# Kernel optimization log

Hardware: AMD Instinct MI355X
Metric: run time of the kernel (lower is better)

The kernel has to match this reference:

```python
import jax, jax.numpy as jnp
import numpy as np
import math

B, S, D, H = 4, 2048, 1024, 16
DK = D // H

def setup_inputs() -> dict:
    key = jax.random.key(0)
    ks = jax.random.split(key, 11)
    mk = lambda k, shape: jax.random.normal(k, shape, dtype=jnp.float32)
    inp = {
        'query': mk(ks[0], (B, S, D)),
        'key':   mk(ks[1], (B, S, D)),
        'value': mk(ks[2], (B, S, D)),
        'Wq': mk(ks[3], (D, D)) * 0.02, 'bq': jnp.zeros((D,), jnp.float32),
        'Wk': mk(ks[4], (D, D)) * 0.02, 'bk': jnp.zeros((D,), jnp.float32),
        'Wv': mk(ks[5], (D, D)) * 0.02, 'bv': jnp.zeros((D,), jnp.float32),
        'Wo': mk(ks[6], (D, D)) * 0.02, 'bo': jnp.zeros((D,), jnp.float32),
    }
    return inp

def reference(query, key, value, Wq, bq, Wk, bk, Wv, bv, Wo, bo):
    b, s, d = query.shape
    scale = 1.0 / math.sqrt(DK)
    def proj(x, W, bias):
        # nn.Linear: x @ W.T + b, then split heads -> [b, h, s, dk]
        return (x @ W.T + bias).reshape(b, s, H, DK).transpose(0, 2, 1, 3)
    q = proj(query, Wq, bq)
    k = proj(key, Wk, bk)
    v = proj(value, Wv, bv)
    scores = jnp.einsum('bhqd,bhkd->bhqk', q, k) * scale  # [b,h,s,s]
    attn = jax.nn.softmax(scores, axis=-1)
    # dropout is identity in eval/reference mode
    x = jnp.einsum('bhqk,bhkd->bhqd', attn, v)
    x = x.transpose(0, 2, 1, 3).reshape(b, s, d)
    return x @ Wo.T + bo
```

## Files before the change

kernel.cpp:

```cpp
#include <hip/hip_runtime.h>
#include <stdint.h>

#define DEV static __device__ __forceinline__

typedef __bf16 bf16_t;
typedef bf16_t bf16x8 __attribute__((ext_vector_type(8)));
typedef bf16_t bf16x4 __attribute__((ext_vector_type(4)));
typedef float f32x4 __attribute__((ext_vector_type(4)));

static constexpr int Bc = 4, Sc = 2048, Dc = 1024, Hc = 16, DKc = 64;
static constexpr int Mrows = Bc * Sc;

DEV unsigned short f2bf(float f) {
  unsigned int u = __float_as_uint(f);
  u += 0x7fffu + ((u >> 16) & 1u);
  return (unsigned short)(u >> 16);
}

DEV float fexp2(float x) {
#if __has_builtin(__builtin_amdgcn_exp2f)
  return __builtin_amdgcn_exp2f(x);
#else
  return exp2f(x);
#endif
}

#if __has_builtin(__builtin_amdgcn_mfma_f32_16x16x16_bf16)
DEV f32x4 mfma16(bf16x4 a, bf16x4 b, f32x4 c) {
  return __builtin_amdgcn_mfma_f32_16x16x16_bf16(a, b, c, 0, 0, 0);
}
#elif __has_builtin(__builtin_amdgcn_mfma_f32_16x16x16bf16_1k)
typedef short s16x4 __attribute__((ext_vector_type(4)));
DEV f32x4 mfma16(bf16x4 a, bf16x4 b, f32x4 c) {
  union U { bf16x4 h; s16x4 s; };
  U ua, ub; ua.h = a; ub.h = b;
  return __builtin_amdgcn_mfma_f32_16x16x16bf16_1k(ua.s, ub.s, c, 0, 0, 0);
}
#else
DEV f32x4 mfma16(bf16x4 a, bf16x4 b, f32x4 c) {
  asm("v_mfma_f32_16x16x16_bf16 %0, %1, %2, %0" : "+v"(c) : "v"(a), "v"(b));
  return c;
}
#endif

DEV void gload_lds16(const void* g, void* l) {
  __builtin_amdgcn_global_load_lds(
      (const __attribute__((address_space(1))) void*)g,
      (__attribute__((address_space(3))) void*)l, 16, 0, 0);
}

__global__ void __launch_bounds__(256) cvt_bf16_seg_kernel(
    const float* __restrict__ s0, const float* __restrict__ s1,
    const float* __restrict__ s2, const float* __restrict__ s3,
    unsigned short* __restrict__ out, int lg) {
  int i = blockIdx.x * blockDim.x + threadIdx.x;
  int seg = i >> lg, j = i & ((1 << lg) - 1);
  const float* src = seg == 0 ? s0 : seg == 1 ? s1 : seg == 2 ? s2 : s3;
  float4 v = reinterpret_cast<const float4*>(src)[j];
  ushort4 o;
  o.x = f2bf(v.x); o.y = f2bf(v.y); o.z = f2bf(v.z); o.w = f2bf(v.w);
  reinterpret_cast<ushort4*>(out)[i] = o;
}

template <int MODE>
__global__ void __launch_bounds__(256) gemm_bt_kernel(
    const unsigned short* __restrict__ A, const unsigned short* __restrict__ W,
    const float* __restrict__ bias, void* __restrict__ Cout,
    int M, int N, int K, float scale) {
  __shared__ unsigned short lA[128 * 64];
  __shared__ unsigned short lB[128 * 64];
  const int t = threadIdx.x;
  const int wv = t >> 6, ln = t & 63;
  const int l15 = ln & 15, lhi = ln >> 4;

  const int nwg = gridDim.x * gridDim.y;
  const int hw = blockIdx.y * gridDim.x + blockIdx.x;
  const int chunk = nwg >> 3;
  const int swzid = (hw & 7) * chunk + (hw >> 3);
  const int m0 = (swzid / gridDim.x) * 128, n0 = (swzid % gridDim.x) * 128;
  const int wr = wv >> 1, wc = wv & 1;
  const int swzR = (l15 & 7) << 4;

  f32x4 acc[4][4] = {};

  for (int k0 = 0; k0 < K; k0 += 64) {
    __syncthreads();
#pragma unroll
    for (int r = 0; r < 4; ++r) {
      int e = r * 2048 + t * 8;
      int row = e >> 6, col = (e & 63) ^ ((row & 7) << 3);
      gload_lds16(A + (size_t)(m0 + row) * K + k0 + col, (char*)lA + e * 2);
      gload_lds16(W + (size_t)(n0 + row) * K + k0 + col, (char*)lB + e * 2);
    }
    __syncthreads();
#pragma unroll
    for (int kk = 0; kk < 2; ++kk) {
      bf16x8 af[4], bfr[4];
#pragma unroll
      for (int i = 0; i < 4; ++i)
        af[i] = *reinterpret_cast<const bf16x8*>(
            (char*)lA + (((wr * 64 + i * 16 + l15) * 128 + kk * 64 + lhi * 16) ^ swzR));
#pragma unroll
      for (int j = 0; j < 4; ++j)
        bfr[j] = *reinterpret_cast<const bf16x8*>(
            (char*)lB + (((wc * 64 + j * 16 + l15) * 128 + kk * 64 + lhi * 16) ^ swzR));
#pragma unroll
      for (int i = 0; i < 4; ++i)
#pragma unroll
        for (int j = 0; j < 4; ++j)
          acc[i][j] = __builtin_amdgcn_mfma_f32_16x16x32_bf16(af[i], bfr[j], acc[i][j], 0, 0, 0);
    }
  }

#pragma unroll
  for (int i = 0; i < 4; ++i)
#pragma unroll
    for (int j = 0; j < 4; ++j) {
      int n = n0 + wc * 64 + j * 16 + l15;
      float bv = bias[n];
      if (MODE == 2) {
        int mb = m0 + wr * 64 + i * 16 + lhi * 4;
        int sl = mb & (Sc - 1);
        int pl = (sl & ~60) | ((sl & 48) >> 2) | ((sl & 12) << 2);
        ushort4 ov;
        ov.x = f2bf((acc[i][j][0] + bv) * scale);
        ov.y = f2bf((acc[i][j][1] + bv) * scale);
        ov.z = f2bf((acc[i][j][2] + bv) * scale);
        ov.w = f2bf((acc[i][j][3] + bv) * scale);
        *reinterpret_cast<ushort4*>((unsigned short*)Cout +
            ((size_t)(mb >> 11) * Dc + n) * Sc + pl) = ov;
      } else {
#pragma unroll
        for (int jj = 0; jj < 4; ++jj) {
          int m = m0 + wr * 64 + i * 16 + lhi * 4 + jj;
          float v = (acc[i][j][jj] + bv) * scale;
          if (MODE == 1)
            ((unsigned short*)Cout)[(size_t)m * N + n] = f2bf(v);
          else
            ((float*)Cout)[(size_t)m * N + n] = v;
        }
      }
    }
}

__global__ void __launch_bounds__(512, 4) attn_kernel(
    const unsigned short* __restrict__ Q, const unsigned short* __restrict__ Kk,
    const unsigned short* __restrict__ Vt, unsigned short* __restrict__ X) {
  __shared__ unsigned short lK[2][64 * 64];
  __shared__ unsigned short lVT[2][64 * 64];
  const int t = threadIdx.x;
  const int wv = t >> 6, ln = t & 63;
  const int l15 = ln & 15, lhi = ln >> 4;
  const int q0 = blockIdx.x * 128;
  const int h = blockIdx.y, b = blockIdx.z;
  const size_t base = (size_t)b * Sc * Dc;
  const int hoff = h * DKc;

  bf16x8 qf[2];
  {
    const unsigned short* qp = Q + base + (size_t)(q0 + wv * 16 + l15) * Dc + hoff + lhi * 8;
    qf[0] = *reinterpret_cast<const bf16x8*>(qp);
    qf[1] = *reinterpret_cast<const bf16x8*>(qp + 32);
  }

  const int e0 = t * 8;
  const int r0 = e0 >> 6, c0 = (e0 & 63) ^ ((r0 & 7) << 3);
  const unsigned short* kS0 = Kk + base + (size_t)r0 * Dc + hoff + c0;
  const unsigned short* vS0 = Vt + ((size_t)b * Dc + hoff + r0) * Sc + c0;

  float mrow = -1e30f;
  f32x4 xacc[4] = {};
  f32x4 lsum = {};
  const int swzK = (l15 & 7) << 4;

  bf16x4 ones4;
#pragma unroll
  for (int i = 0; i < 4; ++i) ones4[i] = (bf16_t)1.0f;

#define STAGE(bi, kv0_)                                                    \
  do {                                                                     \
    gload_lds16(kS0 + (size_t)(kv0_)*Dc, (char*)lK[bi] + e0 * 2);          \
    gload_lds16(vS0 + (kv0_), (char*)lVT[bi] + e0 * 2);                    \
  } while (0)

  STAGE(0, 0);
  asm volatile("s_waitcnt vmcnt(0)" ::: "memory");
  __builtin_amdgcn_s_barrier();
  __builtin_amdgcn_sched_barrier(0);

  for (int tt = 0; tt < Sc / 64; ++tt) {
    const int cur = tt & 1;
    if (tt + 1 < Sc / 64) STAGE(cur ^ 1, (tt + 1) * 64);

    const unsigned short* K_ = lK[cur];
    const unsigned short* VT_ = lVT[cur];

    f32x4 sacc[4];
#pragma unroll
    for (int ct = 0; ct < 4; ++ct) {
      f32x4 z = {};
#pragma unroll
      for (int kk = 0; kk < 2; ++kk) {
        bf16x8 kf = *reinterpret_cast<const bf16x8*>(
            (const char*)K_ + (((ct * 16 + l15) * 128 + kk * 64 + lhi * 16) ^ swzK));
        z = __builtin_amdgcn_mfma_f32_16x16x32_bf16(kf, qf[kk], z, 0, 0, 0);
      }
      sacc[ct] = z;
    }

    float mt = fmaxf(fmaxf(sacc[0][0], sacc[0][1]), fmaxf(sacc[0][2], sacc[0][3]));
#pragma unroll
    for (int ct = 1; ct < 4; ++ct)
      mt = fmaxf(mt,
          fmaxf(fmaxf(sacc[ct][0], sacc[ct][1]), fmaxf(sacc[ct][2], sacc[ct][3])));

    if (__any(mt > mrow + 8.0f)) {
      float mtr = fmaxf(mt, __shfl_xor(mt, 16));
      mtr = fmaxf(mtr, __shfl_xor(mtr, 32));
      float mnew = fmaxf(mrow, mtr);
      float corr = fexp2(mrow - mnew);
      mrow = mnew;
#pragma unroll
      for (int jj = 0; jj < 4; ++jj) {
        float cO = __shfl(corr, lhi * 4 + jj);
        lsum[jj] *= cO;
#pragma unroll
        for (int dt = 0; dt < 4; ++dt) xacc[dt][jj] *= cO;
      }
    }

    bf16x4 pa[4];
#pragma unroll
    for (int ct = 0; ct < 4; ++ct)
#pragma unroll
      for (int jj = 0; jj < 4; ++jj)
        pa[ct][jj] = (bf16_t)fexp2(sacc[ct][jj] - mrow);

#pragma unroll
    for (int ct = 0; ct < 4; ++ct) lsum = mfma16(pa[ct], ones4, lsum);

#pragma unroll
    for (int dt = 0; dt < 4; ++dt) {
#pragma unroll
      for (int sel = 0; sel < 2; ++sel) {
        bf16x8 vb2 = *reinterpret_cast<const bf16x8*>(
            (const char*)VT_ + (((dt * 16 + l15) * 128 + lhi * 32 + sel * 16) ^ swzK));
        bf16x4 vlo = __builtin_shufflevector(vb2, vb2, 0, 1, 2, 3);
        bf16x4 vhi = __builtin_shufflevector(vb2, vb2, 4, 5, 6, 7);
        xacc[dt] = mfma16(pa[2 * sel + 0], vlo, xacc[dt]);
        xacc[dt] = mfma16(pa[2 * sel + 1], vhi, xacc[dt]);
      }
    }

    asm volatile("s_waitcnt vmcnt(0)" ::: "memory");
    __builtin_amdgcn_s_barrier();
    __builtin_amdgcn_sched_barrier(0);
  }
#undef STAGE

  float iO[4];
#pragma unroll
  for (int jj = 0; jj < 4; ++jj) iO[jj] = 1.0f / lsum[jj];

  unsigned short* xp = X + base + (size_t)(q0 + wv * 16) * Dc + hoff;
#pragma unroll
  for (int dt = 0; dt < 4; ++dt)
#pragma unroll
    for (int jj = 0; jj < 4; ++jj) {
      int r = lhi * 4 + jj;
      xp[(size_t)r * Dc + dt * 16 + l15] = f2bf(xacc[dt][jj] * iO[jj]);
    }
}

extern "C" void kernel_launch(void* const* d_in, const int* in_sizes, int n_in,
                              void* d_out, int out_size, void* d_ws, size_t ws_size,
                              hipStream_t stream) {
  const float* query = (const float*)d_in[0];
  const float* key   = (const float*)d_in[1];
  const float* value = (const float*)d_in[2];
  const float* Wq = (const float*)d_in[3];
  const float* bq = (const float*)d_in[4];
  const float* Wk = (const float*)d_in[5];
  const float* bk = (const float*)d_in[6];
  const float* Wv = (const float*)d_in[7];
  const float* bv = (const float*)d_in[8];
  const float* Wo = (const float*)d_in[9];
  const float* bo = (const float*)d_in[10];

  const size_t NBS = (size_t)Mrows * Dc;
  const size_t NW  = (size_t)Dc * Dc;
  unsigned short* bQin = (unsigned short*)d_ws;
  unsigned short* bKin = bQin + NBS;
  unsigned short* bVin = bKin + NBS;
  unsigned short* bWq  = bVin + NBS;
  unsigned short* bWk  = bWq + NW;
  unsigned short* bWv  = bWk + NW;
  unsigned short* bWo  = bWv + NW;
  unsigned short* Qp   = bWo + NW;
  unsigned short* Kp   = Qp + NBS;
  unsigned short* Vtp  = Kp + NBS;
  unsigned short* Xp   = Vtp + NBS;

  cvt_bf16_seg_kernel<<<(int)(3 * NBS / 1024), 256, 0, stream>>>(
      query, key, value, value, bQin, 21);
  cvt_bf16_seg_kernel<<<(int)(4 * NW / 1024), 256, 0, stream>>>(
      Wq, Wk, Wv, Wo, bWq, 18);

  dim3 gg(Dc / 128, Mrows / 128);
  gemm_bt_kernel<1><<<gg, 256, 0, stream>>>(bQin, bWq, bq, Qp, Mrows, Dc, Dc,
                                            0.125f * 1.44269504088896340736f);
  gemm_bt_kernel<1><<<gg, 256, 0, stream>>>(bKin, bWk, bk, Kp, Mrows, Dc, Dc, 1.0f);
  gemm_bt_kernel<2><<<gg, 256, 0, stream>>>(bVin, bWv, bv, Vtp, Mrows, Dc, Dc, 1.0f);

  attn_kernel<<<dim3(Sc / 128, Hc, Bc), 512, 0, stream>>>(Qp, Kp, Vtp, Xp);

  gemm_bt_kernel<0><<<gg, 256, 0, stream>>>(Xp, bWo, bo, d_out, Mrows, Dc, Dc, 1.0f);
}
```

Measured before the change: 237.2 us.

## Double-buffer GEMM LDS tiles and batch QKV projections into one launch

Replaces the single-buffered K=64 GEMM with a double-buffered K=32 pipeline, where the next tile's global-to-LDS loads are issued before the current tile's MFMAs and one barrier is used per iteration. The three Q/K/V projection GEMMs are merged into a single launch indexed by blockIdx.z, which removes two launches and fills the device with more workgroups. LDS usage per block stays the same, but the smaller K step means more barriers and waitcnt stalls per unit of work, and the XOR swizzle is narrowed to 4 rows, which may bring back some bank conflicts.

```diff
diff --git a/kernel.cpp b/kernel.cpp
--- a/kernel.cpp
+++ b/kernel.cpp
@@ -62,16 +62,35 @@
   reinterpret_cast<ushort4*>(out)[i] = o;
 }
 
-template <int MODE>
-__global__ void __launch_bounds__(256) gemm_bt_kernel(
-    const unsigned short* __restrict__ A, const unsigned short* __restrict__ W,
-    const float* __restrict__ bias, void* __restrict__ Cout,
-    int M, int N, int K, float scale) {
-  __shared__ unsigned short lA[128 * 64];
-  __shared__ unsigned short lB[128 * 64];
+template <bool QKV>
+__global__ void __launch_bounds__(256) gemm_dbuf_kernel(
+    const unsigned short* __restrict__ A0, const unsigned short* __restrict__ A1,
+    const unsigned short* __restrict__ A2,
+    const unsigned short* __restrict__ W0, const unsigned short* __restrict__ W1,
+    const unsigned short* __restrict__ W2,
+    const float* __restrict__ b0, const float* __restrict__ b1,
+    const float* __restrict__ b2,
+    void* __restrict__ C0, void* __restrict__ C1, void* __restrict__ C2,
+    int M, int N, int K, float scale0) {
+  __shared__ unsigned short lA[2][128 * 32];
+  __shared__ unsigned short lB[2][128 * 32];
   const int t = threadIdx.x;
   const int wv = t >> 6, ln = t & 63;
   const int l15 = ln & 15, lhi = ln >> 4;
+
+  const unsigned short* A; const unsigned short* W;
+  const float* bias; void* Cout; float scale; int mode;
+  if (QKV) {
+    const int z = blockIdx.z;
+    A = z == 0 ? A0 : z == 1 ? A1 : A2;
+    W = z == 0 ? W0 : z == 1 ? W1 : W2;
+    bias = z == 0 ? b0 : z == 1 ? b1 : b2;
+    Cout = z == 0 ? C0 : z == 1 ? C1 : C2;
+    scale = z == 0 ? scale0 : 1.0f;
+    mode = z == 2 ? 2 : 1;
+  } else {
+    A = A0; W = W0; bias = b0; Cout = C0; scale = scale0; mode = 0;
+  }
 
   const int nwg = gridDim.x * gridDim.y;
   const int hw = blockIdx.y * gridDim.x + blockIdx.x;
@@ -79,38 +98,55 @@
   const int swzid = (hw & 7) * chunk + (hw >> 3);
   const int m0 = (swzid / gridDim.x) * 128, n0 = (swzid % gridDim.x) * 128;
   const int wr = wv >> 1, wc = wv & 1;
-  const int swzR = (l15 & 7) << 4;
+  const int swzR = (l15 & 3) << 4;
+
+  const int rowA = t >> 2;
+  const int colS = ((t & 3) ^ (rowA & 3)) * 8;
+  const unsigned short* aS = A + (size_t)(m0 + rowA) * K + colS;
+  const unsigned short* wS = W + (size_t)(n0 + rowA) * K + colS;
+  const size_t rstep = (size_t)64 * K;
+  const int d0 = t * 16, d1 = 4096 + t * 16;
 
   f32x4 acc[4][4] = {};
 
-  for (int k0 = 0; k0 < K; k0 += 64) {
-    __syncthreads();
-#pragma unroll
-    for (int r = 0; r < 4; ++r) {
-      int e = r * 2048 + t * 8;
-      int row = e >> 6, col = (e & 63) ^ ((row & 7) << 3);
-      gload_lds16(A + (size_t)(m0 + row) * K + k0 + col, (char*)lA + e * 2);
-      gload_lds16(W + (size_t)(n0 + row) * K + k0 + col, (char*)lB + e * 2);
-    }
-    __syncthreads();
-#pragma unroll
-    for (int kk = 0; kk < 2; ++kk) {
-      bf16x8 af[4], bfr[4];
-#pragma unroll
-      for (int i = 0; i < 4; ++i)
-        af[i] = *reinterpret_cast<const bf16x8*>(
-            (char*)lA + (((wr * 64 + i * 16 + l15) * 128 + kk * 64 + lhi * 16) ^ swzR));
+#define GSTAGE(bi, k0_)                                        \
+  do {                                                         \
+    gload_lds16(aS + (k0_), (char*)lA[bi] + d0);               \
+    gload_lds16(aS + rstep + (k0_), (char*)lA[bi] + d1);       \
+    gload_lds16(wS + (k0_), (char*)lB[bi] + d0);               \
+    gload_lds16(wS + rstep + (k0_), (char*)lB[bi] + d1);       \
+  } while (0)
+
+  GSTAGE(0, 0);
+  asm volatile("s_waitcnt vmcnt(0)" ::: "memory");
+  __builtin_amdgcn_s_barrier();
+  __builtin_amdgcn_sched_barrier(0);
+
+  const int NK = K >> 5;
+  for (int tk = 0; tk < NK; ++tk) {
+    const int cur = tk & 1;
+    if (tk + 1 < NK) GSTAGE(cur ^ 1, (tk + 1) * 32);
+
+    bf16x8 af[4], bfr[4];
+#pragma unroll
+    for (int i = 0; i < 4; ++i)
+      af[i] = *reinterpret_cast<const bf16x8*>(
+          (char*)lA[cur] + (((wr * 64 + i * 16 + l15) * 64 + lhi * 16) ^ swzR));
+#pragma unroll
+    for (int j = 0; j < 4; ++j)
+      bfr[j] = *reinterpret_cast<const bf16x8*>(
+          (char*)lB[cur] + (((wc * 64 + j * 16 + l15) * 64 + lhi * 16) ^ swzR));
+#pragma unroll
+    for (int i = 0; i < 4; ++i)
 #pragma unroll
       for (int j = 0; j < 4; ++j)
-        bfr[j] = *reinterpret_cast<const bf16x8*>(
-            (char*)lB + (((wc * 64 + j * 16 + l15) * 128 + kk * 64 + lhi * 16) ^ swzR));
-#pragma unroll
-      for (int i = 0; i < 4; ++i)
-#pragma unroll
-        for (int j = 0; j < 4; ++j)
-          acc[i][j] = __builtin_amdgcn_mfma_f32_16x16x32_bf16(af[i], bfr[j], acc[i][j], 0, 0, 0);
-    }
+        acc[i][j] = __builtin_amdgcn_mfma_f32_16x16x32_bf16(af[i], bfr[j], acc[i][j], 0, 0, 0);
+
+    asm volatile("s_waitcnt vmcnt(0)" ::: "memory");
+    __builtin_amdgcn_s_barrier();
+    __builtin_amdgcn_sched_barrier(0);
   }
+#undef GSTAGE
 
 #pragma unroll
   for (int i = 0; i < 4; ++i)
@@ -118,7 +154,7 @@
     for (int j = 0; j < 4; ++j) {
       int n = n0 + wc * 64 + j * 16 + l15;
       float bv = bias[n];
-      if (MODE == 2) {
+      if (QKV && mode == 2) {
         int mb = m0 + wr * 64 + i * 16 + lhi * 4;
         int sl = mb & (Sc - 1);
         int pl = (sl & ~60) | ((sl & 48) >> 2) | ((sl & 12) << 2);
@@ -134,7 +170,7 @@
         for (int jj = 0; jj < 4; ++jj) {
           int m = m0 + wr * 64 + i * 16 + lhi * 4 + jj;
           float v = (acc[i][j][jj] + bv) * scale;
-          if (MODE == 1)
+          if (QKV)
             ((unsigned short*)Cout)[(size_t)m * N + n] = f2bf(v);
           else
             ((float*)Cout)[(size_t)m * N + n] = v;
@@ -306,13 +342,13 @@
   cvt_bf16_seg_kernel<<<(int)(4 * NW / 1024), 256, 0, stream>>>(
       Wq, Wk, Wv, Wo, bWq, 18);
 
-  dim3 gg(Dc / 128, Mrows / 128);
-  gemm_bt_kernel<1><<<gg, 256, 0, stream>>>(bQin, bWq, bq, Qp, Mrows, Dc, Dc,
-                                            0.125f * 1.44269504088896340736f);
-  gemm_bt_kernel<1><<<gg, 256, 0, stream>>>(bKin, bWk, bk, Kp, Mrows, Dc, Dc, 1.0f);
-  gemm_bt_kernel<2><<<gg, 256, 0, stream>>>(bVin, bWv, bv, Vtp, Mrows, Dc, Dc, 1.0f);
+  gemm_dbuf_kernel<true><<<dim3(Dc / 128, Mrows / 128, 3), 256, 0, stream>>>(
+      bQin, bKin, bVin, bWq, bWk, bWv, bq, bk, bv, Qp, Kp, Vtp,
+      Mrows, Dc, Dc, 0.125f * 1.44269504088896340736f);
 
   attn_kernel<<<dim3(Sc / 128, Hc, Bc), 512, 0, stream>>>(Qp, Kp, Vtp, Xp);
 
-  gemm_bt_kernel<0><<<gg, 256, 0, stream>>>(Xp, bWo, bo, d_out, Mrows, Dc, Dc, 1.0f);
-}
+  gemm_dbuf_kernel<false><<<dim3(Dc / 128, Mrows / 128, 1), 256, 0, stream>>>(
+      Xp, nullptr, nullptr, bWo, nullptr, nullptr, bo, nullptr, nullptr,
+      d_out, nullptr, nullptr, Mrows, Dc, Dc, 1.0f);
+}
```

Result: no change. 234.9 us (-1.0%).
